# Kernel optimization log

Hardware: AMD Instinct MI355X
Metric: run time of the kernel (lower is better)

## Reference

```python
import jax, jax.numpy as jnp
import numpy as np
import math

D = 1024      # input/embed dim
H = 16        # heads
HD = D // H   # head dim
FF = 4096     # feedforward dim
B, S = 2, 2048
LN_EPS = 1e-5
NEG = -9e15


def setup_inputs() -> dict:
    key = jax.random.key(0)
    ks = jax.random.split(key, 16)
    inp = {
        "x": jax.random.normal(ks[0], (B, S, D), jnp.float32),
        "mask": jax.random.randint(ks[1], (1, 1, S, S), 0, 2, jnp.int32),
        "pos_bias": jax.random.normal(ks[2], (1, H, S, S), jnp.float32),
        "sinusoidal_pos": jax.random.normal(ks[3], (1, 1, S, HD), jnp.float32),
        # params (xavier-ish scale)
        "Wqkv": jax.random.normal(ks[4], (D, 3 * D), jnp.float32) * math.sqrt(2.0 / (D + 3 * D)),
        "bqkv": jnp.zeros((3 * D,), jnp.float32),
        "Wo": jax.random.normal(ks[5], (D, D), jnp.float32) * math.sqrt(1.0 / D),
        "bo": jnp.zeros((D,), jnp.float32),
        "W1": jax.random.normal(ks[6], (D, FF), jnp.float32) * math.sqrt(2.0 / (D + FF)),
        "b1": jnp.zeros((FF,), jnp.float32),
        "W2": jax.random.normal(ks[7], (FF, D), jnp.float32) * math.sqrt(2.0 / (D + FF)),
        "b2": jnp.zeros((D,), jnp.float32),
        "g1": jnp.ones((D,), jnp.float32),
        "be1": jnp.zeros((D,), jnp.float32),
        "g2": jnp.ones((D,), jnp.float32),
        "be2": jnp.zeros((D,), jnp.float32),
    }
    return inp


def _layernorm(x, g, b):
    mu = jnp.mean(x, axis=-1, keepdims=True)
    var = jnp.mean(jnp.square(x - mu), axis=-1, keepdims=True)
    return (x - mu) * jax.lax.rsqrt(var + LN_EPS) * g + b


def _rotate_half(x):
    # x: [..., HD] -> reshape [..., 2, HD//2], swap with negation, concat
    r = x.reshape(*x.shape[:-1], 2, -1)
    x1, x2 = r[..., 0, :], r[..., 1, :]
    return jnp.concatenate([-x2, x1], axis=-1)


def _rope(x, sp):
    # sp: [1,1,S,HD]; x: [B,H,S,HD]
    return x * jnp.cos(sp) + _rotate_half(x) * jnp.sin(sp)


def reference(x, mask, pos_bias, sinusoidal_pos, Wqkv, bqkv, Wo, bo,
              W1, b1, W2, b2, g1, be1, g2, be2):
    # pre-norm (note: residual uses the normalized x, matching the source)
    x = _layernorm(x, g1, be1)
    b, s, d = x.shape
    qkv = (x @ Wqkv + bqkv).reshape(b, s, H, 3 * HD).transpose(0, 2, 1, 3)
    q, k, v = jnp.split(qkv, 3, axis=-1)  # each [B,H,S,HD]
    sp = sinusoidal_pos[:, :, -s:]
    q = _rope(q, sp)
    k = _rope(k, sp)
    logits = jnp.einsum("bhqd,bhkd->bhqk", q, k)
    logits = (logits + pos_bias) / math.sqrt(HD)
    logits = jnp.where(mask == 0, NEG, logits)
    attn = jax.nn.softmax(logits, axis=-1)
    vals = jnp.einsum("bhqk,bhkd->bhqd", attn, v)
    vals = vals.transpose(0, 2, 1, 3).reshape(b, s, d)
    attn_out = vals @ Wo + bo
    x = x + attn_out
    x = _layernorm(x, g2, be2)
    h = jax.nn.gelu(x @ W1 + b1, approximate=False)  # torch GELU is exact
    x = x + (h @ W2 + b2)
    return x
```

## Files before the change

kernel.cpp:

```cpp
#include <hip/hip_runtime.h>
#include <math.h>

#define DD   1024
#define HH   16
#define HDD  64
#define FFF  4096
#define NB   2
#define NS   2048
#define NR   (NB * NS)
#define TDQ  (3 * DD)
#define NKT  (NS / 64)

typedef __attribute__((ext_vector_type(8))) _Float16 hfrag;
typedef __attribute__((ext_vector_type(4))) _Float16 h4v;
typedef __attribute__((ext_vector_type(16))) float f32x16;
typedef __attribute__((ext_vector_type(8))) unsigned short us8;
typedef __attribute__((ext_vector_type(4))) unsigned int u32x4;

__device__ __forceinline__ float4 ld4(const float* p) {
    return *reinterpret_cast<const float4*>(p);
}
__device__ __forceinline__ float gelu_f(float x) {
    return 0.5f * x * (1.0f + erff(x * 0.70710678118654752440f));
}
#define MFMA32H(a, b, c) __builtin_amdgcn_mfma_f32_32x32x16_f16((a), (b), (c), 0, 0, 0)

__global__ __launch_bounds__(256) void ln_kernel(const float* __restrict__ in,
        const float* __restrict__ gw, const float* __restrict__ bw,
        float* __restrict__ outf, _Float16* __restrict__ oh) {
    int row = blockIdx.x;
    float4 v = reinterpret_cast<const float4*>(in + (size_t)row * DD)[threadIdx.x];
    float s1 = v.x + v.y + v.z + v.w;
    float s2 = v.x * v.x + v.y * v.y + v.z * v.z + v.w * v.w;
#pragma unroll
    for (int off = 1; off < 64; off <<= 1) {
        s1 += __shfl_xor(s1, off);
        s2 += __shfl_xor(s2, off);
    }
    __shared__ float r1[4], r2[4];
    int wid = threadIdx.x >> 6;
    if ((threadIdx.x & 63) == 0) { r1[wid] = s1; r2[wid] = s2; }
    __syncthreads();
    s1 = r1[0] + r1[1] + r1[2] + r1[3];
    s2 = r2[0] + r2[1] + r2[2] + r2[3];
    float mu   = s1 * (1.0f / DD);
    float var  = s2 * (1.0f / DD) - mu * mu;
    float rstd = rsqrtf(var + 1e-5f);
    float4 g = reinterpret_cast<const float4*>(gw)[threadIdx.x];
    float4 b = reinterpret_cast<const float4*>(bw)[threadIdx.x];
    float o[4];
    o[0] = (v.x - mu) * rstd * g.x + b.x;
    o[1] = (v.y - mu) * rstd * g.y + b.y;
    o[2] = (v.z - mu) * rstd * g.z + b.z;
    o[3] = (v.w - mu) * rstd * g.w + b.w;
    float4 of; of.x = o[0]; of.y = o[1]; of.z = o[2]; of.w = o[3];
    reinterpret_cast<float4*>(outf + (size_t)row * DD)[threadIdx.x] = of;
    h4v hv;
#pragma unroll
    for (int j = 0; j < 4; ++j) hv[j] = (_Float16)o[j];
    *reinterpret_cast<h4v*>(oh + (size_t)row * DD + threadIdx.x * 4) = hv;
}

__global__ __launch_bounds__(256) void wt_convert(const float* __restrict__ W,
        _Float16* __restrict__ Th, int K, int N) {
    __shared__ float s[32][33];
    int tx = threadIdx.x & 31, ty = threadIdx.x >> 5;
    int n0 = blockIdx.x * 32, k0 = blockIdx.y * 32;
#pragma unroll
    for (int i = 0; i < 4; ++i)
        s[ty + i * 8][tx] = W[(size_t)(k0 + ty + i * 8) * N + n0 + tx];
    __syncthreads();
#pragma unroll
    for (int i = 0; i < 4; ++i) {
        int n = n0 + ty + i * 8;
        Th[(size_t)n * K + k0 + tx] = (_Float16)s[tx][ty + i * 8];
    }
}

__global__ __launch_bounds__(256) void cs_table(const float* __restrict__ sp,
        float* __restrict__ ct, float* __restrict__ st) {
    int i = blockIdx.x * 256 + threadIdx.x;
    float v = sp[i];
    ct[i] = cosf(v);
    st[i] = sinf(v);
}

__global__ __launch_bounds__(256) void mask8(const int* __restrict__ mask,
        unsigned char* __restrict__ mb) {
    int i = blockIdx.x * 256 + threadIdx.x;
    int4 v = reinterpret_cast<const int4*>(mask)[i];
    unsigned int o = (unsigned int)(v.x & 1) | ((unsigned int)(v.y & 1) << 8)
                   | ((unsigned int)(v.z & 1) << 16) | ((unsigned int)(v.w & 1) << 24);
    reinterpret_cast<unsigned int*>(mb)[i] = o;
}

__global__ __launch_bounds__(256) void rope_split(const _Float16* __restrict__ qkv,
        const float* __restrict__ ct, const float* __restrict__ st,
        _Float16* __restrict__ Qp, _Float16* __restrict__ Kp, _Float16* __restrict__ Vt) {
    __shared__ _Float16 sv[64][72];
    const int t = threadIdx.x;
    const int tile = blockIdx.x, bh = blockIdx.y;
    const int b = bh >> 4, h = bh & 15;
    const int r = t >> 2, p = t & 3;
    const int srow = tile * 64 + r;
    const _Float16* base = qkv + ((size_t)(b * NS + srow)) * TDQ + h * 192;

#pragma unroll
    for (int qk = 0; qk < 2; ++qk) {
        const _Float16* src = base + qk * 64;
        hfrag va = *reinterpret_cast<const hfrag*>(src + p * 8);
        hfrag vc = *reinterpret_cast<const hfrag*>(src + 32 + p * 8);
        hfrag o1, o2;
#pragma unroll
        for (int j = 0; j < 8; ++j) {
            int d1 = p * 8 + j, d2 = 32 + p * 8 + j;
            float a = (float)va[j], c = (float)vc[j];
            float c1 = ct[(size_t)srow * HDD + d1], s1 = st[(size_t)srow * HDD + d1];
            float c2 = ct[(size_t)srow * HDD + d2], s2 = st[(size_t)srow * HDD + d2];
            o1[j] = (_Float16)(a * c1 - c * s1);
            o2[j] = (_Float16)(c * c2 + a * s2);
        }
        _Float16* dst = qk ? Kp : Qp;
        size_t obase = ((size_t)bh * NS + srow) * HDD;
        *reinterpret_cast<hfrag*>(dst + obase + p * 8)      = o1;
        *reinterpret_cast<hfrag*>(dst + obase + 32 + p * 8) = o2;
    }
    const _Float16* vsrc = base + 128;
    hfrag v0 = *reinterpret_cast<const hfrag*>(vsrc + p * 16);
    hfrag v1 = *reinterpret_cast<const hfrag*>(vsrc + p * 16 + 8);
#pragma unroll
    for (int j = 0; j < 8; ++j) {
        sv[p * 16 + j][r]     = v0[j];
        sv[p * 16 + 8 + j][r] = v1[j];
    }
    __syncthreads();
    {
        int d = t >> 2, kb = (t & 3) * 16;
        size_t obase = ((size_t)bh * HDD + d) * NS + tile * 64 + kb;
        *reinterpret_cast<hfrag*>(Vt + obase)     = *reinterpret_cast<hfrag*>(&sv[d][kb]);
        *reinterpret_cast<hfrag*>(Vt + obase + 8) = *reinterpret_cast<hfrag*>(&sv[d][kb + 8]);
    }
}

__global__ __launch_bounds__(256) void attn_mfma(
        const _Float16* __restrict__ Qp, const _Float16* __restrict__ Kp,
        const _Float16* __restrict__ Vt,
        const float* __restrict__ pos_bias, const unsigned char* __restrict__ maskb,
        float* __restrict__ Opart, float2* __restrict__ Lpart) {
    __shared__ _Float16 kT[64][72];
    __shared__ _Float16 vT[64][72];
    __shared__ _Float16 PBs[4][32][68];
    const int t = threadIdx.x;
    const int w = t >> 6, lane = t & 63, lq = lane & 31, hi = lane >> 5;
    const int h = blockIdx.y >> 1, b = blockIdx.y & 1;
    const int bh = b * HH + h;
    const int qt = blockIdx.x, sp = blockIdx.z;
    const int q0 = qt * 128;
    const int qg = q0 + 32 * w + lq;
    const int sw = ((lq >> 3) & 3) << 3;
    const int KT0 = sp * 16, KT1 = KT0 + 16;
    const float C1  = 0.18033688011112042f;
    const float THR = 11.5f;

    hfrag qf[4];
#pragma unroll
    for (int dk = 0; dk < 4; ++dk)
        qf[dk] = *reinterpret_cast<const hfrag*>(
            Qp + ((size_t)bh * NS + qg) * HDD + 16 * dk + 8 * hi);

    f32x16 o0 = (f32x16)0.0f, o1 = (f32x16)0.0f;
    float mrun = -INFINITY, lsum = 0.0f;

    const int sr0 = t >> 2, sc = t & 3;
    const int swr = ((sr0 >> 3) & 3) << 3;
    const int brow = lane >> 4;
    const int bcol = (lane & 15) * 4;
    us8 kr[2], vr[2];
    float4 pbr[8]; unsigned int pmk[8];

#define STAGE_LOAD(KT) {                                                        \
        int kv0_ = (KT) * 64;                                                   \
        size_t kb_ = ((size_t)bh * NS + kv0_ + sr0) * HDD + 16 * sc;            \
        size_t vb_ = ((size_t)bh * HDD + sr0) * NS + kv0_ + 16 * sc;            \
        kr[0] = *reinterpret_cast<const us8*>(Kp + kb_);                        \
        kr[1] = *reinterpret_cast<const us8*>(Kp + kb_ + 8);                    \
        vr[0] = *reinterpret_cast<const us8*>(Vt + vb_);                        \
        vr[1] = *reinterpret_cast<const us8*>(Vt + vb_ + 8);                    \
        _Pragma("unroll")                                                       \
        for (int i = 0; i < 8; ++i) {                                           \
            int rg_ = q0 + 32 * w + brow + 4 * i;                               \
            pbr[i] = ld4(pos_bias + ((size_t)h * NS + rg_) * NS + kv0_ + bcol); \
            pmk[i] = *reinterpret_cast<const unsigned int*>(                    \
                         maskb + (size_t)rg_ * NS + kv0_ + bcol);               \
        }                                                                       \
    }

    STAGE_LOAD(KT0);
    for (int kt = KT0; kt < KT1; ++kt) {
        __syncthreads();
        *reinterpret_cast<us8*>(&kT[sr0][(16 * sc) ^ swr])     = kr[0];
        *reinterpret_cast<us8*>(&kT[sr0][(16 * sc + 8) ^ swr]) = kr[1];
        *reinterpret_cast<us8*>(&vT[sr0][(16 * sc) ^ swr])     = vr[0];
        *reinterpret_cast<us8*>(&vT[sr0][(16 * sc + 8) ^ swr]) = vr[1];
#pragma unroll
        for (int i = 0; i < 8; ++i) {
            h4v pv;
#pragma unroll
            for (int j = 0; j < 4; ++j)
                pv[j] = ((pmk[i] >> (8 * j)) & 0xffu)
                      ? (_Float16)(pbr[i][j] * C1) : (_Float16)(-60000.0f);
            *reinterpret_cast<h4v*>(&PBs[w][brow + 4 * i][bcol]) = pv;
        }
        __syncthreads();
        if (kt + 1 < KT1) STAGE_LOAD(kt + 1);

        f32x16 s0 = (f32x16)0.0f, s1 = (f32x16)0.0f;
#pragma unroll
        for (int dk = 0; dk < 4; ++dk) {
            hfrag k0 = *reinterpret_cast<const hfrag*>(&kT[lq][(16 * dk + 8 * hi) ^ sw]);
            hfrag k1 = *reinterpret_cast<const hfrag*>(&kT[32 + lq][(16 * dk + 8 * hi) ^ sw]);
            s0 = MFMA32H(k0, qf[dk], s0);
            s1 = MFMA32H(k1, qf[dk], s1);
        }
        float sv[2][16];
#pragma unroll
        for (int m2 = 0; m2 < 2; ++m2)
#pragma unroll
            for (int g = 0; g < 4; ++g) {
                h4v pb4 = *reinterpret_cast<const h4v*>(&PBs[w][lq][32 * m2 + 8 * g + 4 * hi]);
#pragma unroll
                for (int j = 0; j < 4; ++j) {
                    int r = 4 * g + j;
                    float sraw = (m2 == 0) ? s0[r] : s1[r];
                    sv[m2][r] = fmaf(sraw, C1, (float)pb4[j]);
                }
            }
        float mx = sv[0][0];
#pragma unroll
        for (int m2 = 0; m2 < 2; ++m2)
#pragma unroll
            for (int r = 0; r < 16; ++r) mx = fmaxf(mx, sv[m2][r]);
        mx = fmaxf(mx, __shfl_xor(mx, 32));
        if (__any(mx > mrun + THR)) {
            float mnew = fmaxf(mrun, mx);
            float corr = __builtin_amdgcn_exp2f(mrun - mnew);
            lsum *= corr;
            mrun = mnew;
#pragma unroll
            for (int r = 0; r < 16; ++r) {
                int iq = (r & 3) + 8 * (r >> 2) + 4 * hi;
                float cr = __shfl(corr, iq);
                o0[r] *= cr; o1[r] *= cr;
            }
        }
        float ps = 0.0f;
        hfrag af[4];
#pragma unroll
        for (int m2 = 0; m2 < 2; ++m2)
#pragma unroll
            for (int gp = 0; gp < 2; ++gp) {
                float p0 = __builtin_amdgcn_exp2f(sv[m2][8 * gp + 0] - mrun);
                float p1 = __builtin_amdgcn_exp2f(sv[m2][8 * gp + 1] - mrun);
                float p2 = __builtin_amdgcn_exp2f(sv[m2][8 * gp + 2] - mrun);
                float p3 = __builtin_amdgcn_exp2f(sv[m2][8 * gp + 3] - mrun);
                float p4 = __builtin_amdgcn_exp2f(sv[m2][8 * gp + 4] - mrun);
                float p5 = __builtin_amdgcn_exp2f(sv[m2][8 * gp + 5] - mrun);
                float p6 = __builtin_amdgcn_exp2f(sv[m2][8 * gp + 6] - mrun);
                float p7 = __builtin_amdgcn_exp2f(sv[m2][8 * gp + 7] - mrun);
                ps += (p0 + p1) + (p2 + p3) + (p4 + p5) + (p6 + p7);
                unsigned int XA = __builtin_bit_cast(unsigned int, __builtin_amdgcn_cvt_pkrtz(p0, p1));
                unsigned int XB = __builtin_bit_cast(unsigned int, __builtin_amdgcn_cvt_pkrtz(p2, p3));
                unsigned int XC = __builtin_bit_cast(unsigned int, __builtin_amdgcn_cvt_pkrtz(p4, p5));
                unsigned int XD = __builtin_bit_cast(unsigned int, __builtin_amdgcn_cvt_pkrtz(p6, p7));
                unsigned int YA = (unsigned int)__shfl_xor((int)XA, 32);
                unsigned int YB = (unsigned int)__shfl_xor((int)XB, 32);
                unsigned int YC = (unsigned int)__shfl_xor((int)XC, 32);
                unsigned int YD = (unsigned int)__shfl_xor((int)XD, 32);
                u32x4 aw;
                aw[0] = hi ? YC : XA;
                aw[1] = hi ? YD : XB;
                aw[2] = hi ? XC : YA;
                aw[3] = hi ? XD : YB;
                af[m2 * 2 + gp] = __builtin_bit_cast(hfrag, aw);
            }
        ps += __shfl_xor(ps, 32);
        lsum += ps;
#pragma unroll
        for (int kp = 0; kp < 4; ++kp) {
            hfrag v0 = *reinterpret_cast<const hfrag*>(&vT[lq][(16 * kp + 8 * hi) ^ sw]);
            hfrag v1 = *reinterpret_cast<const hfrag*>(&vT[32 + lq][(16 * kp + 8 * hi) ^ sw]);
            o0 = MFMA32H(af[kp], v0, o0);
            o1 = MFMA32H(af[kp], v1, o1);
        }
    }
#undef STAGE_LOAD
    size_t obase = (((size_t)(bh * 16 + qt)) * 2 + sp) * (size_t)(128 * 64);
#pragma unroll
    for (int r = 0; r < 16; ++r) {
        int iq = (r & 3) + 8 * (r >> 2) + 4 * hi;
        Opart[obase + (size_t)(32 * w + iq) * 64 + lq]      = o0[r];
        Opart[obase + (size_t)(32 * w + iq) * 64 + 32 + lq] = o1[r];
    }
    if (hi == 0) {
        float2 ml; ml.x = mrun; ml.y = lsum;
        Lpart[(((size_t)(bh * 16 + qt)) * 2 + sp) * 128 + 32 * w + lq] = ml;
    }
}

__global__ __launch_bounds__(256) void attn_combine(const float* __restrict__ Opart,
        const float2* __restrict__ Lpart, _Float16* __restrict__ valf) {
    const int qt = blockIdx.x;
    const int h = blockIdx.y >> 1, b = blockIdx.y & 1;
    const int bh = b * HH + h;
    const int t = threadIdx.x;
    const int qloc = t >> 2, d0 = (t & 3) * 16;
    size_t base = ((size_t)(bh * 16 + qt)) * 2;
#pragma unroll
    for (int half = 0; half < 2; ++half) {
        int q = qloc + 64 * half;
        float2 ml0 = Lpart[(base + 0) * 128 + q];
        float2 ml1 = Lpart[(base + 1) * 128 + q];
        float m = fmaxf(ml0.x, ml1.x);
        float a0 = __builtin_amdgcn_exp2f(ml0.x - m);
        float a1 = __builtin_amdgcn_exp2f(ml1.x - m);
        float inv = 1.0f / (ml0.y * a0 + ml1.y * a1);
        const float* O0 = Opart + (base + 0) * 8192 + (size_t)q * 64 + d0;
        const float* O1 = Opart + (base + 1) * 8192 + (size_t)q * 64 + d0;
        _Float16* dst = valf + ((size_t)(b * NS + qt * 128 + q)) * DD + h * HDD + d0;
#pragma unroll
        for (int j = 0; j < 4; ++j) {
            float4 x0 = ld4(O0 + 4 * j), x1 = ld4(O1 + 4 * j);
            h4v o;
            o[0] = (_Float16)((x0.x * a0 + x1.x * a1) * inv);
            o[1] = (_Float16)((x0.y * a0 + x1.y * a1) * inv);
            o[2] = (_Float16)((x0.z * a0 + x1.z * a1) * inv);
            o[3] = (_Float16)((x0.w * a0 + x1.w * a1) * inv);
            *reinterpret_cast<h4v*>(dst + 4 * j) = o;
        }
    }
}

template<int EPI>
__global__ __launch_bounds__(256, 2) void gemm_h(
        const _Float16* __restrict__ A, const _Float16* __restrict__ B,
        const float* __restrict__ bias, const float* __restrict__ resid,
        float* __restrict__ Cf, _Float16* __restrict__ Ch,
        int M, int N, int K) {
    __shared__ _Float16 sA[128][72];
    __shared__ _Float16 sB[128][72];
    const int t = threadIdx.x;
    const int w = t >> 6, lane = t & 63, lq = lane & 31, hi = lane >> 5;
    const int wr = w >> 1, wc = w & 1;
    const int m0 = blockIdx.y * 128, n0 = blockIdx.x * 128;
    const int sw = ((lq >> 3) & 3) << 3;

    f32x16 acc[2][2];
#pragma unroll
    for (int m = 0; m < 2; ++m)
#pragma unroll
        for (int n = 0; n < 2; ++n) acc[m][n] = (f32x16)0.0f;

    const int sr = t >> 1, skc = (t & 1) * 16;
    const int swr = ((sr >> 3) & 3) << 3;
    const _Float16* Ap = A + (size_t)(m0 + sr) * K + skc;
    const _Float16* Bp = B + (size_t)(n0 + sr) * K + skc;

    for (int k0 = 0; k0 < K; k0 += 32) {
        us8 a0 = *reinterpret_cast<const us8*>(Ap + k0);
        us8 a1 = *reinterpret_cast<const us8*>(Ap + k0 + 8);
        us8 b0 = *reinterpret_cast<const us8*>(Bp + k0);
        us8 b1 = *reinterpret_cast<const us8*>(Bp + k0 + 8);
        __syncthreads();
        *reinterpret_cast<us8*>(&sA[sr][(skc) ^ swr])     = a0;
        *reinterpret_cast<us8*>(&sA[sr][(skc + 8) ^ swr]) = a1;
        *reinterpret_cast<us8*>(&sB[sr][(skc) ^ swr])     = b0;
        *reinterpret_cast<us8*>(&sB[sr][(skc + 8) ^ swr]) = b1;
        __syncthreads();
        hfrag fa[2][2], fb[2][2];
#pragma unroll
        for (int mb = 0; mb < 2; ++mb)
#pragma unroll
            for (int kc = 0; kc < 2; ++kc)
                fa[mb][kc] = *reinterpret_cast<const hfrag*>(
                    &sA[wr * 64 + mb * 32 + lq][(kc * 16 + 8 * hi) ^ sw]);
#pragma unroll
        for (int nb = 0; nb < 2; ++nb)
#pragma unroll
            for (int kc = 0; kc < 2; ++kc)
                fb[nb][kc] = *reinterpret_cast<const hfrag*>(
                    &sB[wc * 64 + nb * 32 + lq][(kc * 16 + 8 * hi) ^ sw]);
#pragma unroll
        for (int kc = 0; kc < 2; ++kc)
#pragma unroll
            for (int mb = 0; mb < 2; ++mb)
#pragma unroll
                for (int nb = 0; nb < 2; ++nb)
                    acc[mb][nb] = MFMA32H(fa[mb][kc], fb[nb][kc], acc[mb][nb]);
    }
#pragma unroll
    for (int mb = 0; mb < 2; ++mb)
#pragma unroll
        for (int nb = 0; nb < 2; ++nb) {
            int colg = n0 + wc * 64 + nb * 32 + lq;
            float bv = bias[colg];
#pragma unroll
            for (int r = 0; r < 16; ++r) {
                int rowg = m0 + wr * 64 + mb * 32 + (r & 3) + 8 * (r >> 2) + 4 * hi;
                float v = acc[mb][nb][r] + bv;
                if (EPI == 1) v += resid[(size_t)rowg * N + colg];
                if (EPI == 2) {
                    Ch[(size_t)rowg * N + colg] = (_Float16)gelu_f(v);
                } else if (EPI == 3) {
                    Ch[(size_t)rowg * N + colg] = (_Float16)v;
                } else {
                    Cf[(size_t)rowg * N + colg] = v;
                }
            }
        }
}

__global__ __launch_bounds__(256, 2) void gemm_h2(
        const _Float16* __restrict__ A, const _Float16* __restrict__ B,
        const float* __restrict__ bias, const float* __restrict__ resid,
        float* __restrict__ Cf, int M, int N, int K) {
    __shared__ _Float16 sA[64][72];
    __shared__ _Float16 sB[128][72];
    const int t = threadIdx.x;
    const int w = t >> 6, lane = t & 63, lq = lane & 31, hi = lane >> 5;
    const int m0 = blockIdx.y * 64, n0 = blockIdx.x * 128;
    const int sw = ((lq >> 3) & 3) << 3;

    f32x16 acc[2];
    acc[0] = (f32x16)0.0f; acc[1] = (f32x16)0.0f;

    const int ar = t >> 2, akc = (t & 3) * 8;
    const int aswr = ((ar >> 3) & 3) << 3;
    const int br = t >> 1, bkc = (t & 1) * 16;
    const int bswr = ((br >> 3) & 3) << 3;
    const _Float16* Ap = A + (size_t)(m0 + ar) * K + akc;
    const _Float16* Bp = B + (size_t)(n0 + br) * K + bkc;

    for (int k0 = 0; k0 < K; k0 += 32) {
        us8 a0 = *reinterpret_cast<const us8*>(Ap + k0);
        us8 b0 = *reinterpret_cast<const us8*>(Bp + k0);
        us8 b1 = *reinterpret_cast<const us8*>(Bp + k0 + 8);
        __syncthreads();
        *reinterpret_cast<us8*>(&sA[ar][(akc) ^ aswr])     = a0;
        *reinterpret_cast<us8*>(&sB[br][(bkc) ^ bswr])     = b0;
        *reinterpret_cast<us8*>(&sB[br][(bkc + 8) ^ bswr]) = b1;
        __syncthreads();
        hfrag fa[2][2], fb[2];
#pragma unroll
        for (int mb = 0; mb < 2; ++mb)
#pragma unroll
            for (int kc = 0; kc < 2; ++kc)
                fa[mb][kc] = *reinterpret_cast<const hfrag*>(
                    &sA[mb * 32 + lq][(kc * 16 + 8 * hi) ^ sw]);
#pragma unroll
        for (int kc = 0; kc < 2; ++kc)
            fb[kc] = *reinterpret_cast<const hfrag*>(
                &sB[32 * w + lq][(kc * 16 + 8 * hi) ^ sw]);
#pragma unroll
        for (int kc = 0; kc < 2; ++kc)
#pragma unroll
            for (int mb = 0; mb < 2; ++mb)
                acc[mb] = MFMA32H(fa[mb][kc], fb[kc], acc[mb]);
    }
    int colg = n0 + 32 * w + lq;
    float bv = bias[colg];
#pragma unroll
    for (int mb = 0; mb < 2; ++mb)
#pragma unroll
        for (int r = 0; r < 16; ++r) {
            int rowg = m0 + mb * 32 + (r & 3) + 8 * (r >> 2) + 4 * hi;
            float v = acc[mb][r] + bv + resid[(size_t)rowg * N + colg];
            Cf[(size_t)rowg * N + colg] = v;
        }
}

extern "C" void kernel_launch(void* const* d_in, const int* in_sizes, int n_in,
                              void* d_out, int out_size, void* d_ws, size_t ws_size,
                              hipStream_t stream) {
    const float* x        = (const float*)d_in[0];
    const int*   mask     = (const int*)d_in[1];
    const float* pos_bias = (const float*)d_in[2];
    const float* sp       = (const float*)d_in[3];
    const float* Wqkv     = (const float*)d_in[4];
    const float* bqkv     = (const float*)d_in[5];
    const float* Wo       = (const float*)d_in[6];
    const float* bo       = (const float*)d_in[7];
    const float* W1       = (const float*)d_in[8];
    const float* b1       = (const float*)d_in[9];
    const float* W2       = (const float*)d_in[10];
    const float* b2       = (const float*)d_in[11];
    const float* g1       = (const float*)d_in[12];
    const float* be1      = (const float*)d_in[13];
    const float* g2       = (const float*)d_in[14];
    const float* be2      = (const float*)d_in[15];
    float* out = (float*)d_out;
    char* wsb = (char*)d_ws;

    float*          xbuf  = (float*)(wsb);
    _Float16*       actF  = (_Float16*)(wsb + ((size_t)16 << 20));
    _Float16*       wT    = (_Float16*)(wsb + ((size_t)24 << 20));
    float*          ct    = (float*)(wsb + ((size_t)32 << 20));
    float*          stb   = (float*)(wsb + ((size_t)33 << 20));
    unsigned char*  mkb   = (unsigned char*)(wsb + ((size_t)34 << 20));
    _Float16*       qkvh  = (_Float16*)(wsb + ((size_t)48 << 20));
    _Float16*       Qp    = (_Float16*)(wsb + ((size_t)72 << 20));
    _Float16*       Kp    = (_Float16*)(wsb + ((size_t)80 << 20));
    _Float16*       Vt    = (_Float16*)(wsb + ((size_t)88 << 20));
    _Float16*       hF    = (_Float16*)(wsb + ((size_t)48 << 20));
    float*          Opart = (float*)(wsb + ((size_t)96 << 20));
    float2*         Lpart = (float2*)(wsb + ((size_t)130 << 20));

    ln_kernel<<<NR, 256, 0, stream>>>(x, g1, be1, xbuf, actF);
    wt_convert<<<dim3(TDQ / 32, DD / 32), 256, 0, stream>>>(Wqkv, wT, DD, TDQ);
    gemm_h<3><<<dim3(TDQ / 128, NR / 128), 256, 0, stream>>>(
        actF, wT, bqkv, nullptr, nullptr, qkvh, NR, TDQ, DD);
    cs_table<<<(NS * HDD) / 256, 256, 0, stream>>>(sp, ct, stb);
    mask8<<<(NS * NS / 4) / 256, 256, 0, stream>>>(mask, mkb);
    rope_split<<<dim3(NS / 64, NB * HH), 256, 0, stream>>>(qkvh, ct, stb, Qp, Kp, Vt);
    attn_mfma<<<dim3(NS / 128, NB * HH, 2), 256, 0, stream>>>(
        Qp, Kp, Vt, pos_bias, mkb, Opart, Lpart);
    attn_combine<<<dim3(NS / 128, NB * HH), 256, 0, stream>>>(Opart, Lpart, actF);
    wt_convert<<<dim3(DD / 32, DD / 32), 256, 0, stream>>>(Wo, wT, DD, DD);
    gemm_h2<<<dim3(DD / 128, NR / 64), 256, 0, stream>>>(
        actF, wT, bo, xbuf, xbuf, NR, DD, DD);
    ln_kernel<<<NR, 256, 0, stream>>>(xbuf, g2, be2, xbuf, actF);
    wt_convert<<<dim3(FFF / 32, DD / 32), 256, 0, stream>>>(W1, wT, DD, FFF);
    gemm_h<2><<<dim3(FFF / 128, NR / 128), 256, 0, stream>>>(
        actF, wT, b1, nullptr, nullptr, hF, NR, FFF, DD);
    wt_convert<<<dim3(DD / 32, FFF / 32), 256, 0, stream>>>(W2, wT, FFF, DD);
    gemm_h2<<<dim3(DD / 128, NR / 64), 256, 0, stream>>>(
        hF, wT, b2, xbuf, out, NR, DD, FFF);
}
```

Measured before the change: 426.2 us.

## Split attention KV into four chunks, store fp16 partials, prefetch GEMM tiles

```diff
diff --git a/kernel.cpp b/kernel.cpp
--- a/kernel.cpp
+++ b/kernel.cpp
@@ -10,6 +10,7 @@
 #define NR   (NB * NS)
 #define TDQ  (3 * DD)
 #define NKT  (NS / 64)
+#define NSP  4
 
 typedef __attribute__((ext_vector_type(8))) _Float16 hfrag;
 typedef __attribute__((ext_vector_type(4))) _Float16 h4v;
@@ -146,7 +147,7 @@
         const _Float16* __restrict__ Qp, const _Float16* __restrict__ Kp,
         const _Float16* __restrict__ Vt,
         const float* __restrict__ pos_bias, const unsigned char* __restrict__ maskb,
-        float* __restrict__ Opart, float2* __restrict__ Lpart) {
+        _Float16* __restrict__ Opart, float2* __restrict__ Lpart) {
     __shared__ _Float16 kT[64][72];
     __shared__ _Float16 vT[64][72];
     __shared__ _Float16 PBs[4][32][68];
@@ -158,7 +159,7 @@
     const int q0 = qt * 128;
     const int qg = q0 + 32 * w + lq;
     const int sw = ((lq >> 3) & 3) << 3;
-    const int KT0 = sp * 16, KT1 = KT0 + 16;
+    const int KT0 = sp * (NKT / NSP), KT1 = KT0 + (NKT / NSP);
     const float C1  = 0.18033688011112042f;
     const float THR = 11.5f;
 
@@ -215,6 +216,7 @@
         if (kt + 1 < KT1) STAGE_LOAD(kt + 1);
 
         f32x16 s0 = (f32x16)0.0f, s1 = (f32x16)0.0f;
+        __builtin_amdgcn_s_setprio(1);
 #pragma unroll
         for (int dk = 0; dk < 4; ++dk) {
             hfrag k0 = *reinterpret_cast<const hfrag*>(&kT[lq][(16 * dk + 8 * hi) ^ sw]);
@@ -222,6 +224,7 @@
             s0 = MFMA32H(k0, qf[dk], s0);
             s1 = MFMA32H(k1, qf[dk], s1);
         }
+        __builtin_amdgcn_s_setprio(0);
         float sv[2][16];
 #pragma unroll
         for (int m2 = 0; m2 < 2; ++m2)
@@ -285,6 +288,7 @@
             }
         ps += __shfl_xor(ps, 32);
         lsum += ps;
+        __builtin_amdgcn_s_setprio(1);
 #pragma unroll
         for (int kp = 0; kp < 4; ++kp) {
             hfrag v0 = *reinterpret_cast<const hfrag*>(&vT[lq][(16 * kp + 8 * hi) ^ sw]);
@@ -292,51 +296,75 @@
             o0 = MFMA32H(af[kp], v0, o0);
             o1 = MFMA32H(af[kp], v1, o1);
         }
+        __builtin_amdgcn_s_setprio(0);
     }
 #undef STAGE_LOAD
-    size_t obase = (((size_t)(bh * 16 + qt)) * 2 + sp) * (size_t)(128 * 64);
+    float inv = (lsum > 0.0f) ? 1.0f / lsum : 0.0f;
+    size_t obase = (((size_t)(bh * 16 + qt)) * NSP + sp) * (size_t)(128 * 64);
 #pragma unroll
     for (int r = 0; r < 16; ++r) {
         int iq = (r & 3) + 8 * (r >> 2) + 4 * hi;
-        Opart[obase + (size_t)(32 * w + iq) * 64 + lq]      = o0[r];
-        Opart[obase + (size_t)(32 * w + iq) * 64 + 32 + lq] = o1[r];
+        float ivr = __shfl(inv, iq);
+        Opart[obase + (size_t)(32 * w + iq) * 64 + lq]      = (_Float16)(o0[r] * ivr);
+        Opart[obase + (size_t)(32 * w + iq) * 64 + 32 + lq] = (_Float16)(o1[r] * ivr);
     }
     if (hi == 0) {
         float2 ml; ml.x = mrun; ml.y = lsum;
-        Lpart[(((size_t)(bh * 16 + qt)) * 2 + sp) * 128 + 32 * w + lq] = ml;
-    }
-}
-
-__global__ __launch_bounds__(256) void attn_combine(const float* __restrict__ Opart,
+        Lpart[(((size_t)(bh * 16 + qt)) * NSP + sp) * 128 + 32 * w + lq] = ml;
+    }
+}
+
+__global__ __launch_bounds__(256) void attn_combine(const _Float16* __restrict__ Opart,
         const float2* __restrict__ Lpart, _Float16* __restrict__ valf) {
     const int qt = blockIdx.x;
     const int h = blockIdx.y >> 1, b = blockIdx.y & 1;
     const int bh = b * HH + h;
     const int t = threadIdx.x;
-    const int qloc = t >> 2, d0 = (t & 3) * 16;
-    size_t base = ((size_t)(bh * 16 + qt)) * 2;
-#pragma unroll
-    for (int half = 0; half < 2; ++half) {
-        int q = qloc + 64 * half;
-        float2 ml0 = Lpart[(base + 0) * 128 + q];
-        float2 ml1 = Lpart[(base + 1) * 128 + q];
-        float m = fmaxf(ml0.x, ml1.x);
-        float a0 = __builtin_amdgcn_exp2f(ml0.x - m);
-        float a1 = __builtin_amdgcn_exp2f(ml1.x - m);
-        float inv = 1.0f / (ml0.y * a0 + ml1.y * a1);
-        const float* O0 = Opart + (base + 0) * 8192 + (size_t)q * 64 + d0;
-        const float* O1 = Opart + (base + 1) * 8192 + (size_t)q * 64 + d0;
-        _Float16* dst = valf + ((size_t)(b * NS + qt * 128 + q)) * DD + h * HDD + d0;
-#pragma unroll
-        for (int j = 0; j < 4; ++j) {
-            float4 x0 = ld4(O0 + 4 * j), x1 = ld4(O1 + 4 * j);
-            h4v o;
-            o[0] = (_Float16)((x0.x * a0 + x1.x * a1) * inv);
-            o[1] = (_Float16)((x0.y * a0 + x1.y * a1) * inv);
-            o[2] = (_Float16)((x0.z * a0 + x1.z * a1) * inv);
-            o[3] = (_Float16)((x0.w * a0 + x1.w * a1) * inv);
-            *reinterpret_cast<h4v*>(dst + 4 * j) = o;
-        }
+    const int q = t >> 1, dh = (t & 1) * 32;
+    size_t base = ((size_t)(bh * 16 + qt)) * NSP;
+    float2 ml[NSP];
+    float m = -INFINITY;
+#pragma unroll
+    for (int i = 0; i < NSP; ++i) {
+        ml[i] = Lpart[(base + i) * 128 + q];
+        m = fmaxf(m, ml[i].x);
+    }
+    float wgt[NSP], wsum = 0.0f;
+#pragma unroll
+    for (int i = 0; i < NSP; ++i) {
+        wgt[i] = (ml[i].x > -INFINITY) ? ml[i].y * __builtin_amdgcn_exp2f(ml[i].x - m) : 0.0f;
+        wsum += wgt[i];
+    }
+    float inv = (wsum > 0.0f) ? 1.0f / wsum : 0.0f;
+#pragma unroll
+    for (int i = 0; i < NSP; ++i) wgt[i] *= inv;
+    float acc[32];
+#pragma unroll
+    for (int j = 0; j < 32; ++j) acc[j] = 0.0f;
+#pragma unroll
+    for (int i = 0; i < NSP; ++i) {
+        const _Float16* Oi = Opart + (base + i) * 8192 + (size_t)q * 64 + dh;
+        us8 c0 = *reinterpret_cast<const us8*>(Oi);
+        us8 c1 = *reinterpret_cast<const us8*>(Oi + 8);
+        us8 c2 = *reinterpret_cast<const us8*>(Oi + 16);
+        us8 c3 = *reinterpret_cast<const us8*>(Oi + 24);
+        hfrag f0 = __builtin_bit_cast(hfrag, c0), f1 = __builtin_bit_cast(hfrag, c1);
+        hfrag f2 = __builtin_bit_cast(hfrag, c2), f3 = __builtin_bit_cast(hfrag, c3);
+#pragma unroll
+        for (int j = 0; j < 8; ++j) {
+            acc[j]      += (float)f0[j] * wgt[i];
+            acc[8 + j]  += (float)f1[j] * wgt[i];
+            acc[16 + j] += (float)f2[j] * wgt[i];
+            acc[24 + j] += (float)f3[j] * wgt[i];
+        }
+    }
+    _Float16* dst = valf + ((size_t)(b * NS + qt * 128 + q)) * DD + h * HDD + dh;
+#pragma unroll
+    for (int c = 0; c < 4; ++c) {
+        hfrag o;
+#pragma unroll
+        for (int j = 0; j < 8; ++j) o[j] = (_Float16)acc[c * 8 + j];
+        *reinterpret_cast<hfrag*>(dst + c * 8) = o;
     }
 }
 
@@ -365,17 +393,22 @@
     const _Float16* Ap = A + (size_t)(m0 + sr) * K + skc;
     const _Float16* Bp = B + (size_t)(n0 + sr) * K + skc;
 
+    us8 a0, a1, b0, b1;
+#define GEMM_LOAD(KOFF) {                                         \
+        a0 = *reinterpret_cast<const us8*>(Ap + (KOFF));          \
+        a1 = *reinterpret_cast<const us8*>(Ap + (KOFF) + 8);      \
+        b0 = *reinterpret_cast<const us8*>(Bp + (KOFF));          \
+        b1 = *reinterpret_cast<const us8*>(Bp + (KOFF) + 8);      \
+    }
+    GEMM_LOAD(0);
     for (int k0 = 0; k0 < K; k0 += 32) {
-        us8 a0 = *reinterpret_cast<const us8*>(Ap + k0);
-        us8 a1 = *reinterpret_cast<const us8*>(Ap + k0 + 8);
-        us8 b0 = *reinterpret_cast<const us8*>(Bp + k0);
-        us8 b1 = *reinterpret_cast<const us8*>(Bp + k0 + 8);
         __syncthreads();
         *reinterpret_cast<us8*>(&sA[sr][(skc) ^ swr])     = a0;
         *reinterpret_cast<us8*>(&sA[sr][(skc + 8) ^ swr]) = a1;
         *reinterpret_cast<us8*>(&sB[sr][(skc) ^ swr])     = b0;
         *reinterpret_cast<us8*>(&sB[sr][(skc + 8) ^ swr]) = b1;
         __syncthreads();
+        if (k0 + 32 < K) GEMM_LOAD(k0 + 32);
         hfrag fa[2][2], fb[2][2];
 #pragma unroll
         for (int mb = 0; mb < 2; ++mb)
@@ -397,6 +430,7 @@
                 for (int nb = 0; nb < 2; ++nb)
                     acc[mb][nb] = MFMA32H(fa[mb][kc], fb[nb][kc], acc[mb][nb]);
     }
+#undef GEMM_LOAD
 #pragma unroll
     for (int mb = 0; mb < 2; ++mb)
 #pragma unroll
@@ -440,15 +474,20 @@
     const _Float16* Ap = A + (size_t)(m0 + ar) * K + akc;
     const _Float16* Bp = B + (size_t)(n0 + br) * K + bkc;
 
+    us8 a0, b0, b1;
+#define GEMM2_LOAD(KOFF) {                                        \
+        a0 = *reinterpret_cast<const us8*>(Ap + (KOFF));          \
+        b0 = *reinterpret_cast<const us8*>(Bp + (KOFF));          \
+        b1 = *reinterpret_cast<const us8*>(Bp + (KOFF) + 8);      \
+    }
+    GEMM2_LOAD(0);
     for (int k0 = 0; k0 < K; k0 += 32) {
-        us8 a0 = *reinterpret_cast<const us8*>(Ap + k0);
-        us8 b0 = *reinterpret_cast<const us8*>(Bp + k0);
-        us8 b1 = *reinterpret_cast<const us8*>(Bp + k0 + 8);
         __syncthreads();
         *reinterpret_cast<us8*>(&sA[ar][(akc) ^ aswr])     = a0;
         *reinterpret_cast<us8*>(&sB[br][(bkc) ^ bswr])     = b0;
         *reinterpret_cast<us8*>(&sB[br][(bkc + 8) ^ bswr]) = b1;
         __syncthreads();
+        if (k0 + 32 < K) GEMM2_LOAD(k0 + 32);
         hfrag fa[2][2], fb[2];
 #pragma unroll
         for (int mb = 0; mb < 2; ++mb)
@@ -466,6 +505,7 @@
             for (int mb = 0; mb < 2; ++mb)
                 acc[mb] = MFMA32H(fa[mb][kc], fb[kc], acc[mb]);
     }
+#undef GEMM2_LOAD
     int colg = n0 + 32 * w + lq;
     float bv = bias[colg];
 #pragma unroll
@@ -511,8 +551,8 @@
     _Float16*       Kp    = (_Float16*)(wsb + ((size_t)80 << 20));
     _Float16*       Vt    = (_Float16*)(wsb + ((size_t)88 << 20));
     _Float16*       hF    = (_Float16*)(wsb + ((size_t)48 << 20));
-    float*          Opart = (float*)(wsb + ((size_t)96 << 20));
-    float2*         Lpart = (float2*)(wsb + ((size_t)130 << 20));
+    _Float16*       Opart = (_Float16*)(wsb + ((size_t)96 << 20));
+    float2*         Lpart = (float2*)(wsb + ((size_t)128 << 20));
 
     ln_kernel<<<NR, 256, 0, stream>>>(x, g1, be1, xbuf, actF);
     wt_convert<<<dim3(TDQ / 32, DD / 32), 256, 0, stream>>>(Wqkv, wT, DD, TDQ);
@@ -521,7 +561,7 @@
     cs_table<<<(NS * HDD) / 256, 256, 0, stream>>>(sp, ct, stb);
     mask8<<<(NS * NS / 4) / 256, 256, 0, stream>>>(mask, mkb);
     rope_split<<<dim3(NS / 64, NB * HH), 256, 0, stream>>>(qkvh, ct, stb, Qp, Kp, Vt);
-    attn_mfma<<<dim3(NS / 128, NB * HH, 2), 256, 0, stream>>>(
+    attn_mfma<<<dim3(NS / 128, NB * HH, NSP), 256, 0, stream>>>(
         Qp, Kp, Vt, pos_bias, mkb, Opart, Lpart);
     attn_combine<<<dim3(NS / 128, NB * HH), 256, 0, stream>>>(Opart, Lpart, actF);
     wt_convert<<<dim3(DD / 32, DD / 32), 256, 0, stream>>>(Wo, wT, DD, DD);
```

Measured after the change: 428.4 us. No clear change (+0.5%).
